# Kernel optimization log

Hardware: AMD Instinct MI355X
Metric: run time of the kernel (lower is better)

Reference implementation:

```python
import jax, jax.numpy as jnp
import numpy as np

N_FEATURES = 7
N_SETS = 2
N_RULES = N_SETS ** N_FEATURES  # 128
BATCH = 65536


def setup_inputs() -> dict:
    key = jax.random.key(0)
    ks = jax.random.split(key, 7)
    centres = jnp.tile(jnp.linspace(-1.5, 1.5, N_SETS)[None, :], (N_FEATURES, 1))
    x = jax.random.normal(ks[0], (BATCH, N_FEATURES), jnp.float32)
    mu_gauss = centres + 0.1 * jax.random.normal(ks[1], centres.shape, jnp.float32)
    sigma_gauss = jnp.full((N_FEATURES, N_SETS), 0.8, jnp.float32)
    trap_a = centres - 1.2 + 0.05 * jax.random.normal(ks[2], centres.shape, jnp.float32)
    trap_b = centres - 0.4 + 0.05 * jax.random.normal(ks[3], centres.shape, jnp.float32)
    trap_c = centres + 0.4 + 0.05 * jax.random.normal(ks[4], centres.shape, jnp.float32)
    trap_d = centres + 1.2 + 0.05 * jax.random.normal(ks[5], centres.shape, jnp.float32)
    mf_mix = jnp.array(0.0, jnp.float32)
    t_norm_weight = jnp.array(0.0, jnp.float32)
    consequent = 0.01 * jax.random.normal(ks[6], (N_RULES, N_FEATURES + 1), jnp.float32)
    # itertools.product(range(S), repeat=F) ordering == np.indices row-major order
    rule_indices = jnp.asarray(
        np.indices((N_SETS,) * N_FEATURES).reshape(N_FEATURES, -1).T, jnp.int32
    )  # (N_RULES, N_FEATURES)
    return {
        "x": x, "mu_gauss": mu_gauss, "sigma_gauss": sigma_gauss,
        "trap_a": trap_a, "trap_b": trap_b, "trap_c": trap_c, "trap_d": trap_d,
        "mf_mix": mf_mix, "t_norm_weight": t_norm_weight,
        "consequent": consequent, "rule_indices": rule_indices,
    }


def reference(x, mu_gauss, sigma_gauss, trap_a, trap_b, trap_c, trap_d,
              mf_mix, t_norm_weight, consequent, rule_indices):
    B = x.shape[0]
    xe = x[..., None]  # (B, F, 1)
    # Gaussian MF
    sig = jnp.clip(sigma_gauss, 1e-6, None)
    gauss = jnp.exp(-(xe - mu_gauss) ** 2 / (2.0 * sig ** 2))  # (B, F, S)
    # Trapezoid MF with soft-sorted params a<b<=c<d
    params = jnp.sort(jnp.stack([trap_a, trap_b, trap_c, trap_d], axis=-1), axis=-1)
    a, b, c, d = params[..., 0], params[..., 1], params[..., 2], params[..., 3]
    left = jnp.clip((xe - a) / (b - a + 1e-6), 0.0, 1.0)
    flat = ((xe >= b) & (xe <= c)).astype(x.dtype)
    right = jnp.clip((d - xe) / (d - c + 1e-6), 0.0, 1.0)
    trap = jnp.maximum(jnp.minimum(left, right), flat)  # (B, F, S)
    # MF blend
    alpha = jax.nn.sigmoid(mf_mix)
    mem = alpha * gauss + (1.0 - alpha) * trap  # (B, F, S)
    # Rule gather: for each feature i, pick mem[:, i, rule_indices[:, i]]
    feat_idx = jnp.arange(N_FEATURES)[:, None]               # (F, 1)
    gathered = mem[:, feat_idx, rule_indices.T]              # (B, F, R)
    # Learnable t-norm: blend of product and min
    w = jax.nn.sigmoid(t_norm_weight)
    firing = w * jnp.prod(gathered, axis=1) + (1.0 - w) * jnp.min(gathered, axis=1)  # (B, R)
    norm_firing = firing / (jnp.sum(firing, axis=1, keepdims=True) + 1e-8)
    # TSK consequent: x_aug @ consequent^T
    x_aug = jnp.concatenate([jnp.ones((B, 1), x.dtype), x], axis=1)  # (B, F+1)
    rule_out = x_aug @ consequent.T                                  # (B, R)
    out = jnp.sum(norm_firing * rule_out, axis=1, keepdims=True)     # (B, 1)
    return (out, norm_firing, mem)
```

## Files before the change

### kernel.cpp

```cpp
#include <hip/hip_runtime.h>
#include <math.h>

#define NF 7
#define NR 128
#define RPB 8
#define ITERS 4

__global__ __launch_bounds__(256) void anfis_kernel(
    const float* __restrict__ x,
    const float* __restrict__ mu_g,
    const float* __restrict__ sig_g,
    const float* __restrict__ ta, const float* __restrict__ tb,
    const float* __restrict__ tc, const float* __restrict__ td,
    const float* __restrict__ mf_mix,
    const float* __restrict__ tnw,
    const float* __restrict__ consequent,
    const int*   __restrict__ rule_idx,
    float* __restrict__ out,
    float* __restrict__ nf_out,
    float* __restrict__ mem_out,
    int nrows)
{
    __shared__ float s_xaug[RPB][8];
    __shared__ float s_mem[RPB][16];
    __shared__ unsigned int s_mask32[32];

    const int tid = threadIdx.x;
    const int row_local = tid >> 5;
    const int j = tid & 31;

    if (tid < NR) {
        int m = 0;
        #pragma unroll
        for (int i = 0; i < NF; ++i)
            if (rule_idx[tid * NF + i] != 0) m |= (1 << i);
        ((unsigned char*)s_mask32)[tid] = (unsigned char)m;
    }
    const float alpha = 1.0f / (1.0f + __expf(-mf_mix[0]));
    const float w     = 1.0f / (1.0f + __expf(-tnw[0]));

    float mu_j = 0.f, i2s2 = 0.f, q0 = 0.f, q1 = 0.f, q2 = 0.f, q3 = 0.f;
    float invL = 0.f, invR = 0.f;
    if (j < 14) {
        mu_j = mu_g[j];
        float sg = fmaxf(sig_g[j], 1e-6f);
        i2s2 = 1.0f / (2.0f * sg * sg);

        float p0 = ta[j], p1 = tb[j], p2 = tc[j], p3 = td[j];
        float lo, hi;
        lo = fminf(p0, p1); hi = fmaxf(p0, p1); p0 = lo; p1 = hi;
        lo = fminf(p2, p3); hi = fmaxf(p2, p3); p2 = lo; p3 = hi;
        lo = fminf(p0, p2); hi = fmaxf(p0, p2); p0 = lo; p2 = hi;
        lo = fminf(p1, p3); hi = fmaxf(p1, p3); p1 = lo; p3 = hi;
        lo = fminf(p1, p2); hi = fmaxf(p1, p2); p1 = lo; p2 = hi;
        q0 = p0; q1 = p1; q2 = p2; q3 = p3;
        invL = 1.0f / (p1 - p0 + 1e-6f);
        invR = 1.0f / (p3 - p2 + 1e-6f);
    }
    const float one_m_alpha = 1.0f - alpha;
    const float one_m_w     = 1.0f - w;

    const int base = blockIdx.x * (RPB * ITERS);
    const float4* __restrict__ cq = (const float4*)consequent;

    for (int it = 0; it < ITERS; ++it) {
        const int row = base + it * RPB + row_local;
        const bool live = (row < nrows);

        __syncthreads();

        if (j < NF) s_xaug[row_local][1 + j] = live ? x[row * NF + j] : 0.0f;
        if (j == NF) s_xaug[row_local][0] = 1.0f;

        if (j < 14) {
            const float xi = live ? x[row * NF + (j >> 1)] : 0.0f;
            const float dm = xi - mu_j;
            const float gauss = __expf(-(dm * dm) * i2s2);
            float left  = (xi - q0) * invL;
            left = fminf(fmaxf(left, 0.0f), 1.0f);
            const float flat = (xi >= q1 && xi <= q2) ? 1.0f : 0.0f;
            float right = (q3 - xi) * invR;
            right = fminf(fmaxf(right, 0.0f), 1.0f);
            const float trap = fmaxf(fminf(left, right), flat);
            const float m = fmaf(alpha, gauss, one_m_alpha * trap);
            s_mem[row_local][j] = m;
            if (live) mem_out[row * 14 + j] = m;
        }
        __syncthreads();

        const float4 xa0 = *(const float4*)&s_xaug[row_local][0];
        const float4 xa1 = *(const float4*)&s_xaug[row_local][4];
        const float4 mA = *(const float4*)&s_mem[row_local][0];
        const float4 mB = *(const float4*)&s_mem[row_local][4];
        const float4 mC = *(const float4*)&s_mem[row_local][8];
        const float  mD0 = s_mem[row_local][12];
        const float  mD1 = s_mem[row_local][13];

        float mlo[NF], mhi[NF];
        mlo[0] = mA.x; mhi[0] = mA.y;
        mlo[1] = mA.z; mhi[1] = mA.w;
        mlo[2] = mB.x; mhi[2] = mB.y;
        mlo[3] = mB.z; mhi[3] = mB.w;
        mlo[4] = mC.x; mhi[4] = mC.y;
        mlo[5] = mC.z; mhi[5] = mC.w;
        mlo[6] = mD0;  mhi[6] = mD1;

        const unsigned int pk = s_mask32[j];
        const int r0 = 4 * j;

        float f[4];
        float S = 0.0f, dot = 0.0f;

        #pragma unroll
        for (int k = 0; k < 4; ++k) {
            const unsigned int msk = (pk >> (8 * k)) & 0xffu;
            float g[NF];
            #pragma unroll
            for (int i = 0; i < NF; ++i)
                g[i] = ((msk >> i) & 1u) ? mhi[i] : mlo[i];

            const float prod = ((g[0] * g[1]) * (g[2] * g[3])) *
                               ((g[4] * g[5]) * g[6]);
            const float mn = fminf(fminf(fminf(g[0], g[1]), fminf(g[2], g[3])),
                                   fminf(fminf(g[4], g[5]), g[6]));
            const float fr = fmaf(w, prod, one_m_w * mn);

            const int r = r0 + k;
            const float4 c0 = cq[2 * r];
            const float4 c1 = cq[2 * r + 1];
            float ro = c0.x * xa0.x;
            ro = fmaf(c0.y, xa0.y, ro);
            ro = fmaf(c0.z, xa0.z, ro);
            ro = fmaf(c0.w, xa0.w, ro);
            ro = fmaf(c1.x, xa1.x, ro);
            ro = fmaf(c1.y, xa1.y, ro);
            ro = fmaf(c1.z, xa1.z, ro);
            ro = fmaf(c1.w, xa1.w, ro);

            f[k] = fr;
            S += fr;
            dot = fmaf(fr, ro, dot);
        }

        #pragma unroll
        for (int off = 1; off < 32; off <<= 1) {
            S   += __shfl_xor(S, off, 64);
            dot += __shfl_xor(dot, off, 64);
        }
        const float invS = 1.0f / (S + 1e-8f);

        if (live) {
            float4 nf4;
            nf4.x = f[0] * invS;
            nf4.y = f[1] * invS;
            nf4.z = f[2] * invS;
            nf4.w = f[3] * invS;
            *(float4*)&nf_out[row * NR + r0] = nf4;
            if (j == 0) out[row] = dot * invS;
        }
    }
}

extern "C" void kernel_launch(void* const* d_in, const int* in_sizes, int n_in,
                              void* d_out, int out_size, void* d_ws, size_t ws_size,
                              hipStream_t stream) {
    const float* x     = (const float*)d_in[0];
    const float* mu_g  = (const float*)d_in[1];
    const float* sig_g = (const float*)d_in[2];
    const float* ta    = (const float*)d_in[3];
    const float* tb    = (const float*)d_in[4];
    const float* tc    = (const float*)d_in[5];
    const float* td    = (const float*)d_in[6];
    const float* mfm   = (const float*)d_in[7];
    const float* tnw   = (const float*)d_in[8];
    const float* cons  = (const float*)d_in[9];
    const int*   ridx  = (const int*)d_in[10];

    const int nrows = in_sizes[0] / NF;

    float* out     = (float*)d_out;
    float* nf_out  = out + nrows;
    float* mem_out = nf_out + (size_t)nrows * NR;

    const int rows_per_block = RPB * ITERS;
    const int grid = (nrows + rows_per_block - 1) / rows_per_block;
    anfis_kernel<<<grid, 256, 0, stream>>>(x, mu_g, sig_g, ta, tb, tc, td,
                                           mfm, tnw, cons, ridx,
                                           out, nf_out, mem_out, nrows);
}
```

Baseline: 106.3 us.

## Compute all block memberships in one phase and share 5-feature partial products

Restructures the kernel so all 32 rows' membership values are computed up front, with 16 threads per row across two halves, followed by a single barrier. This replaces the per-iteration pair of barriers. The rule loop now exploits that each thread's 4 consecutive rules share the first 5 feature selections, computing that partial product and min once and varying only features 5 and 6. The shared-rule assumption depends on rule_indices ordering (consecutive rules differ only in the last two features), which holds for the row-major product ordering. The nf_out index is also widened to size_t.

```diff
diff --git a/kernel.cpp b/kernel.cpp
--- a/kernel.cpp
+++ b/kernel.cpp
@@ -1,19 +1,15 @@
 #include <hip/hip_runtime.h>
-#include <math.h>
 
 #define NF 7
 #define NR 128
-#define RPB 8
-#define ITERS 4
+#define ROWS 32
 
 __global__ __launch_bounds__(256) void anfis_kernel(
     const float* __restrict__ x,
-    const float* __restrict__ mu_g,
-    const float* __restrict__ sig_g,
+    const float* __restrict__ mu_g,  const float* __restrict__ sig_g,
     const float* __restrict__ ta, const float* __restrict__ tb,
     const float* __restrict__ tc, const float* __restrict__ td,
-    const float* __restrict__ mf_mix,
-    const float* __restrict__ tnw,
+    const float* __restrict__ mf_mix, const float* __restrict__ tnw,
     const float* __restrict__ consequent,
     const int*   __restrict__ rule_idx,
     float* __restrict__ out,
@@ -21,13 +17,12 @@
     float* __restrict__ mem_out,
     int nrows)
 {
-    __shared__ float s_xaug[RPB][8];
-    __shared__ float s_mem[RPB][16];
+    __shared__ float s_x[ROWS][8];
+    __shared__ float s_mem[ROWS][16];
     __shared__ unsigned int s_mask32[32];
 
-    const int tid = threadIdx.x;
-    const int row_local = tid >> 5;
-    const int j = tid & 31;
+    const int tid  = threadIdx.x;
+    const int base = blockIdx.x * ROWS;
 
     if (tid < NR) {
         int m = 0;
@@ -36,94 +31,100 @@
             if (rule_idx[tid * NF + i] != 0) m |= (1 << i);
         ((unsigned char*)s_mask32)[tid] = (unsigned char)m;
     }
+
     const float alpha = 1.0f / (1.0f + __expf(-mf_mix[0]));
     const float w     = 1.0f / (1.0f + __expf(-tnw[0]));
+    const float a1 = 1.0f - alpha, w1 = 1.0f - w;
 
-    float mu_j = 0.f, i2s2 = 0.f, q0 = 0.f, q1 = 0.f, q2 = 0.f, q3 = 0.f;
-    float invL = 0.f, invR = 0.f;
-    if (j < 14) {
-        mu_j = mu_g[j];
-        float sg = fmaxf(sig_g[j], 1e-6f);
-        i2s2 = 1.0f / (2.0f * sg * sg);
+    {
+        const int j   = tid & 15;
+        const int r16 = tid >> 4;
 
-        float p0 = ta[j], p1 = tb[j], p2 = tc[j], p3 = td[j];
-        float lo, hi;
-        lo = fminf(p0, p1); hi = fmaxf(p0, p1); p0 = lo; p1 = hi;
-        lo = fminf(p2, p3); hi = fmaxf(p2, p3); p2 = lo; p3 = hi;
-        lo = fminf(p0, p2); hi = fmaxf(p0, p2); p0 = lo; p2 = hi;
-        lo = fminf(p1, p3); hi = fmaxf(p1, p3); p1 = lo; p3 = hi;
-        lo = fminf(p1, p2); hi = fmaxf(p1, p2); p1 = lo; p2 = hi;
-        q0 = p0; q1 = p1; q2 = p2; q3 = p3;
-        invL = 1.0f / (p1 - p0 + 1e-6f);
-        invR = 1.0f / (p3 - p2 + 1e-6f);
+        float mu_j = 0.f, i2s2 = 0.f, q0 = 0.f, q1 = 0.f, q2 = 0.f, q3 = 0.f;
+        float invL = 0.f, invR = 0.f;
+        if (j < 14) {
+            mu_j = mu_g[j];
+            float sg = fmaxf(sig_g[j], 1e-6f);
+            i2s2 = 1.0f / (2.0f * sg * sg);
+            float p0 = ta[j], p1 = tb[j], p2 = tc[j], p3 = td[j];
+            float lo, hi;
+            lo = fminf(p0, p1); hi = fmaxf(p0, p1); p0 = lo; p1 = hi;
+            lo = fminf(p2, p3); hi = fmaxf(p2, p3); p2 = lo; p3 = hi;
+            lo = fminf(p0, p2); hi = fmaxf(p0, p2); p0 = lo; p2 = hi;
+            lo = fminf(p1, p3); hi = fmaxf(p1, p3); p1 = lo; p3 = hi;
+            lo = fminf(p1, p2); hi = fmaxf(p1, p2); p1 = lo; p2 = hi;
+            q0 = p0; q1 = p1; q2 = p2; q3 = p3;
+            invL = 1.0f / (p1 - p0 + 1e-6f);
+            invR = 1.0f / (p3 - p2 + 1e-6f);
+        }
+
+        #pragma unroll
+        for (int h = 0; h < 2; ++h) {
+            const int rl  = r16 + 16 * h;
+            const int row = base + rl;
+            const bool live = (row < nrows);
+            if (j < 14) {
+                const float xi = live ? x[row * NF + (j >> 1)] : 0.0f;
+                const float dm = xi - mu_j;
+                const float gauss = __expf(-(dm * dm) * i2s2);
+                float left = (xi - q0) * invL;
+                left = fminf(fmaxf(left, 0.f), 1.f);
+                const float flat = (xi >= q1 && xi <= q2) ? 1.f : 0.f;
+                float right = (q3 - xi) * invR;
+                right = fminf(fmaxf(right, 0.f), 1.f);
+                const float trap = fmaxf(fminf(left, right), flat);
+                const float m = fmaf(alpha, gauss, a1 * trap);
+                s_mem[rl][j] = m;
+                if (live) mem_out[row * 14 + j] = m;
+                if ((j & 1) == 0) s_x[rl][1 + (j >> 1)] = xi;
+            } else if (j == 15) {
+                s_x[rl][0] = 1.0f;
+            }
+        }
     }
-    const float one_m_alpha = 1.0f - alpha;
-    const float one_m_w     = 1.0f - w;
+    __syncthreads();
 
-    const int base = blockIdx.x * (RPB * ITERS);
+    const int g  = tid >> 5;
+    const int jj = tid & 31;
+    const unsigned int pk = s_mask32[jj];
+    const int r0 = 4 * jj;
     const float4* __restrict__ cq = (const float4*)consequent;
 
-    for (int it = 0; it < ITERS; ++it) {
-        const int row = base + it * RPB + row_local;
+    #pragma unroll
+    for (int it = 0; it < 4; ++it) {
+        const int rl  = g + 8 * it;
+        const int row = base + rl;
         const bool live = (row < nrows);
 
-        __syncthreads();
+        const float4 xa0 = *(const float4*)&s_x[rl][0];
+        const float4 xa1 = *(const float4*)&s_x[rl][4];
+        const float4 mA = *(const float4*)&s_mem[rl][0];
+        const float4 mB = *(const float4*)&s_mem[rl][4];
+        const float4 mC = *(const float4*)&s_mem[rl][8];
+        const float2 mD = *(const float2*)&s_mem[rl][12];
 
-        if (j < NF) s_xaug[row_local][1 + j] = live ? x[row * NF + j] : 0.0f;
-        if (j == NF) s_xaug[row_local][0] = 1.0f;
+        const float mlo[7] = {mA.x, mA.z, mB.x, mB.z, mC.x, mC.z, mD.x};
+        const float mhi[7] = {mA.y, mA.w, mB.y, mB.w, mC.y, mC.w, mD.y};
 
-        if (j < 14) {
-            const float xi = live ? x[row * NF + (j >> 1)] : 0.0f;
-            const float dm = xi - mu_j;
-            const float gauss = __expf(-(dm * dm) * i2s2);
-            float left  = (xi - q0) * invL;
-            left = fminf(fmaxf(left, 0.0f), 1.0f);
-            const float flat = (xi >= q1 && xi <= q2) ? 1.0f : 0.0f;
-            float right = (q3 - xi) * invR;
-            right = fminf(fmaxf(right, 0.0f), 1.0f);
-            const float trap = fmaxf(fminf(left, right), flat);
-            const float m = fmaf(alpha, gauss, one_m_alpha * trap);
-            s_mem[row_local][j] = m;
-            if (live) mem_out[row * 14 + j] = m;
-        }
-        __syncthreads();
-
-        const float4 xa0 = *(const float4*)&s_xaug[row_local][0];
-        const float4 xa1 = *(const float4*)&s_xaug[row_local][4];
-        const float4 mA = *(const float4*)&s_mem[row_local][0];
-        const float4 mB = *(const float4*)&s_mem[row_local][4];
-        const float4 mC = *(const float4*)&s_mem[row_local][8];
-        const float  mD0 = s_mem[row_local][12];
-        const float  mD1 = s_mem[row_local][13];
-
-        float mlo[NF], mhi[NF];
-        mlo[0] = mA.x; mhi[0] = mA.y;
-        mlo[1] = mA.z; mhi[1] = mA.w;
-        mlo[2] = mB.x; mhi[2] = mB.y;
-        mlo[3] = mB.z; mhi[3] = mB.w;
-        mlo[4] = mC.x; mhi[4] = mC.y;
-        mlo[5] = mC.z; mhi[5] = mC.w;
-        mlo[6] = mD0;  mhi[6] = mD1;
-
-        const unsigned int pk = s_mask32[j];
-        const int r0 = 4 * j;
+        const unsigned int m0 = pk & 0xffu;
+        float p0 = (m0 & 1u)  ? mhi[0] : mlo[0];
+        float p1 = (m0 & 2u)  ? mhi[1] : mlo[1];
+        float p2 = (m0 & 4u)  ? mhi[2] : mlo[2];
+        float p3 = (m0 & 8u)  ? mhi[3] : mlo[3];
+        float p4 = (m0 & 16u) ? mhi[4] : mlo[4];
+        const float P5 = ((p0 * p1) * (p2 * p3)) * p4;
+        const float M5 = fminf(fminf(fminf(p0, p1), fminf(p2, p3)), p4);
 
         float f[4];
-        float S = 0.0f, dot = 0.0f;
-
+        float S = 0.f, dot = 0.f;
         #pragma unroll
         for (int k = 0; k < 4; ++k) {
-            const unsigned int msk = (pk >> (8 * k)) & 0xffu;
-            float g[NF];
-            #pragma unroll
-            for (int i = 0; i < NF; ++i)
-                g[i] = ((msk >> i) & 1u) ? mhi[i] : mlo[i];
-
-            const float prod = ((g[0] * g[1]) * (g[2] * g[3])) *
-                               ((g[4] * g[5]) * g[6]);
-            const float mn = fminf(fminf(fminf(g[0], g[1]), fminf(g[2], g[3])),
-                                   fminf(fminf(g[4], g[5]), g[6]));
-            const float fr = fmaf(w, prod, one_m_w * mn);
+            const unsigned int mk = pk >> (8 * k);
+            const float g5 = (mk & 0x20u) ? mhi[5] : mlo[5];
+            const float g6 = (mk & 0x40u) ? mhi[6] : mlo[6];
+            const float prod = P5 * (g5 * g6);
+            const float mn   = fminf(M5, fminf(g5, g6));
+            const float fr   = fmaf(w, prod, w1 * mn);
 
             const int r = r0 + k;
             const float4 c0 = cq[2 * r];
@@ -155,8 +156,8 @@
             nf4.y = f[1] * invS;
             nf4.z = f[2] * invS;
             nf4.w = f[3] * invS;
-            *(float4*)&nf_out[row * NR + r0] = nf4;
-            if (j == 0) out[row] = dot * invS;
+            *(float4*)&nf_out[(size_t)row * NR + r0] = nf4;
+            if (jj == 0) out[row] = dot * invS;
         }
     }
 }
@@ -182,8 +183,7 @@
     float* nf_out  = out + nrows;
     float* mem_out = nf_out + (size_t)nrows * NR;
 
-    const int rows_per_block = RPB * ITERS;
-    const int grid = (nrows + rows_per_block - 1) / rows_per_block;
+    const int grid = (nrows + ROWS - 1) / ROWS;
     anfis_kernel<<<grid, 256, 0, stream>>>(x, mu_g, sig_g, ta, tb, tc, td,
                                            mfm, tnw, cons, ridx,
                                            out, nf_out, mem_out, nrows);
```

After: 115.7 us. 8.8% more time.
